# Optimization experiments

Hardware: AMD Instinct MI355X
Metric: run time of the kernel (lower is better)

## Reference

```python
import jax, jax.numpy as jnp
import numpy as np

N_NODES = 50000
N_EDGES = 600000
IN_C = 128
HID = 128
OUT_C = 32
N_GRAPHS = 64


def setup_inputs() -> dict:
    key = jax.random.key(0)
    ks = jax.random.split(key, 12)
    x = jax.random.normal(ks[0], (N_NODES, IN_C), dtype=jnp.float32)
    edge_index = jax.random.randint(ks[1], (2, N_EDGES), 0, N_NODES, dtype=jnp.int64)
    batch = jnp.sort(jax.random.randint(ks[2], (N_NODES,), 0, N_GRAPHS, dtype=jnp.int64))
    s1 = 1.0 / np.sqrt(IN_C)
    s2 = 1.0 / np.sqrt(HID)
    # SAGEConv: out = lin_l(mean_neighbors) + lin_r(x); lin_l has bias, lin_r has none
    W1l = jax.random.uniform(ks[3], (HID, IN_C), minval=-s1, maxval=s1, dtype=jnp.float32)
    b1 = jax.random.uniform(ks[4], (HID,), minval=-s1, maxval=s1, dtype=jnp.float32)
    W1r = jax.random.uniform(ks[5], (HID, IN_C), minval=-s1, maxval=s1, dtype=jnp.float32)
    W2l = jax.random.uniform(ks[6], (HID, HID), minval=-s2, maxval=s2, dtype=jnp.float32)
    b2 = jax.random.uniform(ks[7], (HID,), minval=-s2, maxval=s2, dtype=jnp.float32)
    W2r = jax.random.uniform(ks[8], (HID, HID), minval=-s2, maxval=s2, dtype=jnp.float32)
    Wlin = jax.random.uniform(ks[9], (OUT_C, HID), minval=-s2, maxval=s2, dtype=jnp.float32)
    blin = jax.random.uniform(ks[10], (OUT_C,), minval=-s2, maxval=s2, dtype=jnp.float32)
    return {"x": x, "edge_index": edge_index, "batch": batch,
            "W1l": W1l, "b1": b1, "W1r": W1r,
            "W2l": W2l, "b2": b2, "W2r": W2r,
            "Wlin": Wlin, "blin": blin}


def _sage_conv(x, src, dst, Wl, bl, Wr):
    # mean aggregation of source-node features onto destination nodes
    msg_sum = jax.ops.segment_sum(x[src], dst, num_segments=N_NODES)  # [N, d]
    deg = jax.ops.segment_sum(jnp.ones((src.shape[0],), x.dtype), dst, num_segments=N_NODES)
    mean = msg_sum / jnp.maximum(deg, 1.0)[:, None]
    return mean @ Wl.T + bl + x @ Wr.T


def reference(x, edge_index, batch, W1l, b1, W1r, W2l, b2, W2r, Wlin, blin):
    src, dst = edge_index[0], edge_index[1]
    h = jax.nn.relu(_sage_conv(x, src, dst, W1l, b1, W1r))
    h = jax.nn.relu(_sage_conv(h, src, dst, W2l, b2, W2r))
    # global mean pool over graph ids
    gsum = jax.ops.segment_sum(h, batch, num_segments=N_GRAPHS)        # [G, HID]
    cnt = jax.ops.segment_sum(jnp.ones((h.shape[0],), h.dtype), batch, num_segments=N_GRAPHS)
    pooled = gsum / jnp.maximum(cnt, 1.0)[:, None]
    return pooled @ Wlin.T + blin
```

## Files before the change

### kernel.cpp

```cpp
#include <hip/hip_runtime.h>
#include <hip/hip_fp16.h>

#define N_NODES 50000
#define N_EDGES 600000
#define N_GRAPHS 64
#define HID 128
#define OUT_C 32

#define N_SCAN_BLOCKS ((N_NODES + 255) / 256)
#define SCAN_FLAG 0x40000000

typedef __attribute__((ext_vector_type(8))) _Float16 half8;
typedef __attribute__((ext_vector_type(4))) float f32x4;

#define ZERO_INTS (2 * N_NODES + N_SCAN_BLOCKS + N_GRAPHS * HID)

__global__ __launch_bounds__(256) void zero_kernel(int* __restrict__ zb) {
    int i = blockIdx.x * 256 + threadIdx.x;
    if (i < ZERO_INTS) zb[i] = 0;
}

#define DEG_BLOCKS ((N_EDGES + 255) / 256)
#define GST_BLOCKS ((N_NODES + 256) / 256)

__global__ __launch_bounds__(256) void deg_gst_w(
    const int* __restrict__ dst, int* __restrict__ degi,
    const int* __restrict__ batch, int* __restrict__ gstart,
    const float* __restrict__ W1l, const float* __restrict__ W1r,
    const float* __restrict__ W2l, const float* __restrict__ W2r,
    __half* __restrict__ Wt1, __half* __restrict__ Wt2) {
    const int b = blockIdx.x;
    const int t = threadIdx.x;
    if (b < DEG_BLOCKS) {
        int e = b * 256 + t;
        if (e < N_EDGES) atomicAdd(&degi[dst[e]], 1);
    } else if (b < DEG_BLOCKS + GST_BLOCKS) {
        int i = (b - DEG_BLOCKS) * 256 + t;
        if (i <= N_NODES) {
            if (i == 0) {
                int b1 = batch[0];
                for (int g = 0; g <= b1; ++g) gstart[g] = 0;
            } else if (i == N_NODES) {
                int b0 = batch[N_NODES - 1];
                for (int g = b0 + 1; g <= N_GRAPHS; ++g) gstart[g] = N_NODES;
            } else {
                int b0 = batch[i - 1], b1 = batch[i];
                for (int g = b0 + 1; g <= b1; ++g) gstart[g] = i;
            }
        }
    } else {
        int local = (b - DEG_BLOCKS - GST_BLOCKS) * 256 + t;
        for (int i = local; i < 65536; i += 4096) {
            int which = i >> 15;
            int j = i & 32767;
            int n = j >> 8, k = j & 255;
            const float* Wl = which ? W2l : W1l;
            const float* Wr = which ? W2r : W1r;
            float a = (k < 128) ? Wl[n * 128 + k] : Wr[n * 128 + (k - 128)];
            (which ? Wt2 : Wt1)[j] = __float2half(a);
        }
    }
}

__global__ __launch_bounds__(256) void scan_fused(
    const int* __restrict__ deg, int* __restrict__ bsum,
    int* __restrict__ rowptr, float* __restrict__ invdeg) {
    __shared__ int s[256];
    const int b = blockIdx.x;
    const int t = threadIdx.x;
    const int idx = b * 256 + t;
    const int v = (idx < N_NODES) ? deg[idx] : 0;
    s[t] = v;
    __syncthreads();
    for (int off = 1; off < 256; off <<= 1) {
        int u = (t >= off) ? s[t - off] : 0;
        __syncthreads();
        s[t] += u;
        __syncthreads();
    }
    const int incl = s[t];
    if (t == 255) atomicExch(&bsum[b], incl | SCAN_FLAG);

    int pv = 0;
    if (t < b) {
        int w;
        do { w = atomicAdd(&bsum[t], 0); } while (!(w & SCAN_FLAG));
        pv = w & ~SCAN_FLAG;
    }
    __syncthreads();
    s[t] = pv;
    __syncthreads();
    for (int off = 128; off > 0; off >>= 1) {
        if (t < off) s[t] += s[t + off];
        __syncthreads();
    }
    const int boffs = s[0];

    if (idx < N_NODES) {
        rowptr[idx] = boffs + incl - v;
        invdeg[idx] = 1.0f / fmaxf((float)v, 1.0f);
    }
    if (b == N_SCAN_BLOCKS - 1 && t == 255) rowptr[N_NODES] = boffs + incl;
}

__global__ __launch_bounds__(256) void fill_cast(
    const int* __restrict__ src, const int* __restrict__ dst,
    const int* __restrict__ rowptr, int* __restrict__ cursor,
    int* __restrict__ eidx,
    const float* __restrict__ x, __half* __restrict__ xh) {
    const int b = blockIdx.x;
    const int t = threadIdx.x;
    if (b < DEG_BLOCKS) {
        int e = b * 256 + t;
        if (e < N_EDGES) {
            int d = dst[e];
            int pos = atomicAdd(&cursor[d], 1);
            eidx[rowptr[d] + pos] = src[e];
        }
    } else {
        int i = ((b - DEG_BLOCKS) * 256 + t) * 4;
        if (i < N_NODES * 128) {
            float4 v = *(const float4*)(x + i);
            __half2 a = __floats2half2_rn(v.x, v.y);
            __half2 c = __floats2half2_rn(v.z, v.w);
            uint2 st;
            st.x = *(const unsigned int*)&a;
            st.y = *(const unsigned int*)&c;
            *(uint2*)(xh + i) = st;
        }
    }
}

#define GBM 64

__global__ __launch_bounds__(256, 2) void sage_fused(
    const __half* __restrict__ feat16, const int* __restrict__ rowptr,
    const int* __restrict__ eidx, const float* __restrict__ invdeg,
    const __half* __restrict__ Wt, const float* __restrict__ bias,
    __half* __restrict__ out16,
    const int* __restrict__ batch, float* __restrict__ pooled,
    int M, int do_pool) {
    __shared__ __align__(16) __half Bs[128 * 256];
    __shared__ __align__(16) __half Ms[64 * 128];

    const int tid = threadIdx.x;
    const int wave = tid >> 6;
    const int lane = tid & 63;
    const int l15 = lane & 15;
    const int quad = lane >> 4;
    const int row0 = blockIdx.x * GBM;

    for (int id = tid; id < 128 * 32; id += 256) {
        int n = id >> 5;
        int kc16 = (id & 31) * 16;
        int off = (n * 512 + kc16) ^ ((n & 7) << 4);
        *(half8*)((char*)Bs + off) = *(const half8*)((const char*)Wt + n * 512 + kc16);
    }

    const int g16 = tid >> 4;
    const int sub = tid & 15;
    const int gbase = lane & 48;
    const size_t coff = (size_t)sub * 8;

    int begq[4], endq[4], pre0q[4], pre1q[4];
#pragma unroll
    for (int q = 0; q < 4; ++q) {
        int node = row0 + g16 + 16 * q;
        int bq = 0, eq = 0;
        if (node < M) { bq = rowptr[node]; eq = rowptr[node + 1]; }
        begq[q] = bq; endq[q] = eq;
    }
#pragma unroll
    for (int q = 0; q < 4; ++q) {
        int bq = begq[q], eq = endq[q];
        pre0q[q] = (eq > bq) ? eidx[min(bq + sub,      eq - 1)] : 0;
        pre1q[q] = (eq > bq) ? eidx[min(bq + 16 + sub, eq - 1)] : 0;
    }

#pragma unroll
    for (int q = 0; q < 4; ++q) {
        const int nloc = g16 + 16 * q;
        const int node = row0 + nloc;
        const int beg = begq[q], end = endq[q];
        const int deg = end - beg;

        float4 a[4], bb[4];
#pragma unroll
        for (int g = 0; g < 4; ++g) { a[g] = (float4){0.f,0.f,0.f,0.f}; bb[g] = (float4){0.f,0.f,0.f,0.f}; }

        for (int j0 = 0; j0 < deg; j0 += 16) {
            int idx[16];
            if (j0 == 0) {
#pragma unroll
                for (int k = 0; k < 16; ++k) idx[k] = __shfl(pre0q[q], gbase + k);
            } else if (j0 == 16) {
#pragma unroll
                for (int k = 0; k < 16; ++k) idx[k] = __shfl(pre1q[q], gbase + k);
            } else {
#pragma unroll
                for (int k = 0; k < 16; ++k) idx[k] = eidx[min(beg + j0 + k, end - 1)];
            }
            half8 v[16];
#pragma unroll
            for (int k = 0; k < 16; ++k)
                v[k] = *(const half8*)(feat16 + (size_t)idx[k] * 128 + coff);
            const int rem = deg - j0;
#pragma unroll
            for (int k = 0; k < 16; ++k) {
                const float w = (k < rem) ? 1.0f : 0.0f;
                const int g = k & 3;
                a[g].x  += w * (float)v[k][0];
                a[g].y  += w * (float)v[k][1];
                a[g].z  += w * (float)v[k][2];
                a[g].w  += w * (float)v[k][3];
                bb[g].x += w * (float)v[k][4];
                bb[g].y += w * (float)v[k][5];
                bb[g].z += w * (float)v[k][6];
                bb[g].w += w * (float)v[k][7];
            }
        }

        const float sc = (node < M) ? invdeg[node] : 1.0f;
        half8 r;
        r[0] = (_Float16)(((a[0].x + a[1].x) + (a[2].x + a[3].x)) * sc);
        r[1] = (_Float16)(((a[0].y + a[1].y) + (a[2].y + a[3].y)) * sc);
        r[2] = (_Float16)(((a[0].z + a[1].z) + (a[2].z + a[3].z)) * sc);
        r[3] = (_Float16)(((a[0].w + a[1].w) + (a[2].w + a[3].w)) * sc);
        r[4] = (_Float16)(((bb[0].x + bb[1].x) + (bb[2].x + bb[3].x)) * sc);
        r[5] = (_Float16)(((bb[0].y + bb[1].y) + (bb[2].y + bb[3].y)) * sc);
        r[6] = (_Float16)(((bb[0].z + bb[1].z) + (bb[2].z + bb[3].z)) * sc);
        r[7] = (_Float16)(((bb[0].w + bb[1].w) + (bb[2].w + bb[3].w)) * sc);
        int moff = (nloc * 256 + (int)sub * 16) ^ ((nloc & 7) << 4);
        *(half8*)((char*)Ms + moff) = r;
    }

    __syncthreads();

    const int arow = wave * 16 + l15;
    const int gi_a = min(row0 + arow, M - 1);
    half8 af[8];
#pragma unroll
    for (int kb = 0; kb < 4; ++kb) {
        int off = (arow * 256 + kb * 64 + quad * 16) ^ ((arow & 7) << 4);
        af[kb] = *(const half8*)((const char*)Ms + off);
    }
#pragma unroll
    for (int kb = 4; kb < 8; ++kb) {
        af[kb] = *(const half8*)(feat16 + (size_t)gi_a * 128 + (kb - 4) * 32 + quad * 8);
    }

    f32x4 acc[8];
#pragma unroll
    for (int t = 0; t < 8; ++t) acc[t] = (f32x4){0.f, 0.f, 0.f, 0.f};

#pragma unroll
    for (int kb = 0; kb < 8; ++kb) {
#pragma unroll
        for (int t = 0; t < 8; ++t) {
            const int n = t * 16 + l15;
            const int boff = (n * 512 + kb * 64 + quad * 16) ^ ((n & 7) << 4);
            const half8 b = *(const half8*)((const char*)Bs + boff);
            acc[t] = __builtin_amdgcn_mfma_f32_16x16x32_f16(af[kb], b, acc[t], 0, 0, 0);
        }
    }

    if (!do_pool) {
#pragma unroll
        for (int r = 0; r < 4; ++r) {
            int gi = row0 + wave * 16 + quad * 4 + r;
            if (gi < M) {
#pragma unroll
                for (int t = 0; t < 8; ++t) {
                    int col = t * 16 + l15;
                    float v = fmaxf(acc[t][r] + bias[col], 0.f);
                    out16[(size_t)gi * 128 + col] = __float2half(v);
                }
            }
        }
    } else {
        __syncthreads();
#pragma unroll
        for (int r = 0; r < 4; ++r) {
            int lrow = wave * 16 + quad * 4 + r;
            int gi = row0 + lrow;
#pragma unroll
            for (int t = 0; t < 8; ++t) {
                int col = t * 16 + l15;
                float v = fmaxf(acc[t][r] + bias[col], 0.f);
                if (gi >= M) v = 0.f;
                int off = (lrow * 256 + col * 2) ^ ((lrow & 7) << 4);
                *(__half*)((char*)Ms + off) = __float2half(v);
            }
        }
        __syncthreads();
        if (tid < 128) {
            const int col = tid;
            int cur = batch[min(row0, M - 1)];
            float s = 0.f;
            for (int r = 0; r < 64; ++r) {
                int gr = batch[min(row0 + r, M - 1)];
                if (gr != cur) {
                    atomicAdd(&pooled[cur * 128 + col], s);
                    s = 0.f; cur = gr;
                }
                int off = (r * 256 + col * 2) ^ ((r & 7) << 4);
                s += __half2float(*(const __half*)((const char*)Ms + off));
            }
            atomicAdd(&pooled[cur * 128 + col], s);
        }
    }
}

__global__ void final_kernel(const float* __restrict__ pooled,
                             const int* __restrict__ gstart,
                             const float* __restrict__ Wlin, const float* __restrict__ blin,
                             float* __restrict__ out) {
    int g = blockIdx.x;
    int j = threadIdx.x;
    float inv = 1.0f / fmaxf((float)(gstart[g + 1] - gstart[g]), 1.0f);
    float sum = blin[j];
    const float* w = Wlin + j * 128;
    const float* p = pooled + (size_t)g * 128;
    for (int c = 0; c < 128; ++c) {
        sum += p[c] * inv * w[c];
    }
    out[g * 32 + j] = sum;
}

extern "C" void kernel_launch(void* const* d_in, const int* in_sizes, int n_in,
                              void* d_out, int out_size, void* d_ws, size_t ws_size,
                              hipStream_t stream) {
    const float* x    = (const float*)d_in[0];
    const int*   src  = (const int*)d_in[1];
    const int*   dst  = ((const int*)d_in[1]) + N_EDGES;
    const int*   batch= (const int*)d_in[2];
    const float* W1l  = (const float*)d_in[3];
    const float* b1   = (const float*)d_in[4];
    const float* W1r  = (const float*)d_in[5];
    const float* W2l  = (const float*)d_in[6];
    const float* b2   = (const float*)d_in[7];
    const float* W2r  = (const float*)d_in[8];
    const float* Wlin = (const float*)d_in[9];
    const float* blin = (const float*)d_in[10];
    float* out = (float*)d_out;

    __half* xh     = (__half*)d_ws;
    __half* h1_16  = xh + 6400000;
    __half* Wt1    = h1_16 + 6400000;
    __half* Wt2    = Wt1 + 32768;
    float* invdeg  = (float*)(Wt2 + 32768);
    int*   gstart  = (int*)(invdeg + N_NODES);
    int*   degi    = gstart + 65;
    int*   cursor  = degi + N_NODES;
    int*   bsum    = cursor + N_NODES;
    float* pooled  = (float*)(bsum + N_SCAN_BLOCKS);
    int*   rowptr  = (int*)(pooled + N_GRAPHS*HID);
    int*   eidx    = rowptr + N_NODES + 1;

    zero_kernel<<<(ZERO_INTS + 255) / 256, 256, 0, stream>>>(degi);

    deg_gst_w<<<DEG_BLOCKS + GST_BLOCKS + 16, 256, 0, stream>>>(
        dst, degi, batch, gstart, W1l, W1r, W2l, W2r, Wt1, Wt2);

    scan_fused<<<N_SCAN_BLOCKS, 256, 0, stream>>>(degi, bsum, rowptr, invdeg);

    fill_cast<<<DEG_BLOCKS + (N_NODES * 128 / 4 + 255) / 256, 256, 0, stream>>>(
        src, dst, rowptr, cursor, eidx, x, xh);

    const int grid = (N_NODES + GBM - 1) / GBM;

    sage_fused<<<grid, 256, 0, stream>>>(
        xh, rowptr, eidx, invdeg, Wt1, b1, h1_16, batch, pooled, N_NODES, 0);

    sage_fused<<<grid, 256, 0, stream>>>(
        h1_16, rowptr, eidx, invdeg, Wt2, b2, (__half*)0, batch, pooled, N_NODES, 1);

    final_kernel<<<N_GRAPHS, 32, 0, stream>>>(pooled, gstart, Wlin, blin, out);
}
```

Before: 250.5 us.

## Make SAGE layers persistent with atomic 16-row tile scheduling; simplify scan lookback

Replaces the one-block-per-64-rows SAGE kernel with a persistent kernel of 512 blocks. Each block stages the weight matrix in LDS once, then pulls 16-row tiles from a global atomic counter, so weight loading is amortised and uneven node degrees are load-balanced dynamically. Each wave now computes 2 of the 8 output column tiles for a shared 16-row A tile. The scan kernel's decoupled lookback is also reduced to a single wave polling with sleep and a shuffle reduction, replacing the 256-thread LDS tree. Costs are an extra atomic and barrier per tile and smaller tiles per iteration. In the pooling path, output is written into the shared Ms buffer with no barrier after the A-fragment reads, so there is a possible cross-wave race.

```diff
diff --git a/kernel.cpp b/kernel.cpp
--- a/kernel.cpp
+++ b/kernel.cpp
@@ -9,11 +9,13 @@
 
 #define N_SCAN_BLOCKS ((N_NODES + 255) / 256)
 #define SCAN_FLAG 0x40000000
+#define N_TILES (N_NODES / 16)
+#define SAGE_BLOCKS 512
 
 typedef __attribute__((ext_vector_type(8))) _Float16 half8;
 typedef __attribute__((ext_vector_type(4))) float f32x4;
 
-#define ZERO_INTS (2 * N_NODES + N_SCAN_BLOCKS + N_GRAPHS * HID)
+#define ZERO_INTS (2 * N_NODES + N_SCAN_BLOCKS + N_GRAPHS * HID + 2)
 
 __global__ __launch_bounds__(256) void zero_kernel(int* __restrict__ zb) {
     int i = blockIdx.x * 256 + threadIdx.x;
@@ -82,18 +84,18 @@
     if (t == 255) atomicExch(&bsum[b], incl | SCAN_FLAG);
 
     int pv = 0;
-    if (t < b) {
-        int w;
-        do { w = atomicAdd(&bsum[t], 0); } while (!(w & SCAN_FLAG));
-        pv = w & ~SCAN_FLAG;
+    if (t < 64) {
+        for (int f = t; f < b; f += 64) {
+            int w;
+            while (!((w = atomicAdd(&bsum[f], 0)) & SCAN_FLAG)) {
+                __builtin_amdgcn_s_sleep(2);
+            }
+            pv += w & ~SCAN_FLAG;
+        }
+        for (int off = 32; off > 0; off >>= 1) pv += __shfl_down(pv, off);
+        if (t == 0) s[0] = pv;
     }
     __syncthreads();
-    s[t] = pv;
-    __syncthreads();
-    for (int off = 128; off > 0; off >>= 1) {
-        if (t < off) s[t] += s[t + off];
-        __syncthreads();
-    }
     const int boffs = s[0];
 
     if (idx < N_NODES) {
@@ -131,24 +133,22 @@
     }
 }
 
-#define GBM 64
-
-__global__ __launch_bounds__(256, 2) void sage_fused(
+__global__ __launch_bounds__(256, 2) void sage_persist(
     const __half* __restrict__ feat16, const int* __restrict__ rowptr,
     const int* __restrict__ eidx, const float* __restrict__ invdeg,
     const __half* __restrict__ Wt, const float* __restrict__ bias,
     __half* __restrict__ out16,
     const int* __restrict__ batch, float* __restrict__ pooled,
-    int M, int do_pool) {
+    int* __restrict__ ctr, int do_pool) {
     __shared__ __align__(16) __half Bs[128 * 256];
-    __shared__ __align__(16) __half Ms[64 * 128];
+    __shared__ __align__(16) __half Ms[16 * 128];
+    __shared__ int sTile;
 
     const int tid = threadIdx.x;
     const int wave = tid >> 6;
     const int lane = tid & 63;
     const int l15 = lane & 15;
     const int quad = lane >> 4;
-    const int row0 = blockIdx.x * GBM;
 
     for (int id = tid; id < 128 * 32; id += 256) {
         int n = id >> 5;
@@ -162,27 +162,19 @@
     const int gbase = lane & 48;
     const size_t coff = (size_t)sub * 8;
 
-    int begq[4], endq[4], pre0q[4], pre1q[4];
-#pragma unroll
-    for (int q = 0; q < 4; ++q) {
-        int node = row0 + g16 + 16 * q;
-        int bq = 0, eq = 0;
-        if (node < M) { bq = rowptr[node]; eq = rowptr[node + 1]; }
-        begq[q] = bq; endq[q] = eq;
-    }
-#pragma unroll
-    for (int q = 0; q < 4; ++q) {
-        int bq = begq[q], eq = endq[q];
-        pre0q[q] = (eq > bq) ? eidx[min(bq + sub,      eq - 1)] : 0;
-        pre1q[q] = (eq > bq) ? eidx[min(bq + 16 + sub, eq - 1)] : 0;
-    }
-
-#pragma unroll
-    for (int q = 0; q < 4; ++q) {
-        const int nloc = g16 + 16 * q;
-        const int node = row0 + nloc;
-        const int beg = begq[q], end = endq[q];
+    for (;;) {
+        if (tid == 0) sTile = atomicAdd(ctr, 1);
+        __syncthreads();
+        const int tile = sTile;
+        if (tile >= N_TILES) break;
+        const int row0 = tile * 16;
+
+        const int node = row0 + g16;
+        const int beg = rowptr[node];
+        const int end = rowptr[node + 1];
         const int deg = end - beg;
+        const int pre0 = (deg > 0) ? eidx[min(beg + sub,      end - 1)] : 0;
+        const int pre1 = (deg > 0) ? eidx[min(beg + 16 + sub, end - 1)] : 0;
 
         float4 a[4], bb[4];
 #pragma unroll
@@ -192,10 +184,10 @@
             int idx[16];
             if (j0 == 0) {
 #pragma unroll
-                for (int k = 0; k < 16; ++k) idx[k] = __shfl(pre0q[q], gbase + k);
+                for (int k = 0; k < 16; ++k) idx[k] = __shfl(pre0, gbase + k);
             } else if (j0 == 16) {
 #pragma unroll
-                for (int k = 0; k < 16; ++k) idx[k] = __shfl(pre1q[q], gbase + k);
+                for (int k = 0; k < 16; ++k) idx[k] = __shfl(pre1, gbase + k);
             } else {
 #pragma unroll
                 for (int k = 0; k < 16; ++k) idx[k] = eidx[min(beg + j0 + k, end - 1)];
@@ -220,7 +212,7 @@
             }
         }
 
-        const float sc = (node < M) ? invdeg[node] : 1.0f;
+        const float sc = invdeg[node];
         half8 r;
         r[0] = (_Float16)(((a[0].x + a[1].x) + (a[2].x + a[3].x)) * sc);
         r[1] = (_Float16)(((a[0].y + a[1].y) + (a[2].y + a[3].y)) * sc);
@@ -230,83 +222,76 @@
         r[5] = (_Float16)(((bb[0].y + bb[1].y) + (bb[2].y + bb[3].y)) * sc);
         r[6] = (_Float16)(((bb[0].z + bb[1].z) + (bb[2].z + bb[3].z)) * sc);
         r[7] = (_Float16)(((bb[0].w + bb[1].w) + (bb[2].w + bb[3].w)) * sc);
-        int moff = (nloc * 256 + (int)sub * 16) ^ ((nloc & 7) << 4);
+        int moff = (g16 * 256 + (int)sub * 16) ^ ((g16 & 7) << 4);
         *(half8*)((char*)Ms + moff) = r;
-    }
-
-    __syncthreads();
-
-    const int arow = wave * 16 + l15;
-    const int gi_a = min(row0 + arow, M - 1);
-    half8 af[8];
-#pragma unroll
-    for (int kb = 0; kb < 4; ++kb) {
-        int off = (arow * 256 + kb * 64 + quad * 16) ^ ((arow & 7) << 4);
-        af[kb] = *(const half8*)((const char*)Ms + off);
-    }
-#pragma unroll
-    for (int kb = 4; kb < 8; ++kb) {
-        af[kb] = *(const half8*)(feat16 + (size_t)gi_a * 128 + (kb - 4) * 32 + quad * 8);
-    }
-
-    f32x4 acc[8];
-#pragma unroll
-    for (int t = 0; t < 8; ++t) acc[t] = (f32x4){0.f, 0.f, 0.f, 0.f};
-
-#pragma unroll
-    for (int kb = 0; kb < 8; ++kb) {
-#pragma unroll
-        for (int t = 0; t < 8; ++t) {
-            const int n = t * 16 + l15;
-            const int boff = (n * 512 + kb * 64 + quad * 16) ^ ((n & 7) << 4);
-            const half8 b = *(const half8*)((const char*)Bs + boff);
-            acc[t] = __builtin_amdgcn_mfma_f32_16x16x32_f16(af[kb], b, acc[t], 0, 0, 0);
-        }
-    }
-
-    if (!do_pool) {
-#pragma unroll
-        for (int r = 0; r < 4; ++r) {
-            int gi = row0 + wave * 16 + quad * 4 + r;
-            if (gi < M) {
-#pragma unroll
-                for (int t = 0; t < 8; ++t) {
-                    int col = t * 16 + l15;
-                    float v = fmaxf(acc[t][r] + bias[col], 0.f);
+
+        __syncthreads();
+
+        half8 af[8];
+#pragma unroll
+        for (int kb = 0; kb < 4; ++kb) {
+            int off = (l15 * 256 + kb * 64 + quad * 16) ^ ((l15 & 7) << 4);
+            af[kb] = *(const half8*)((const char*)Ms + off);
+        }
+#pragma unroll
+        for (int kb = 4; kb < 8; ++kb) {
+            af[kb] = *(const half8*)(feat16 + (size_t)(row0 + l15) * 128 + (kb - 4) * 32 + quad * 8);
+        }
+
+        f32x4 acc[2];
+        acc[0] = (f32x4){0.f, 0.f, 0.f, 0.f};
+        acc[1] = (f32x4){0.f, 0.f, 0.f, 0.f};
+#pragma unroll
+        for (int tt = 0; tt < 2; ++tt) {
+            const int n = (wave * 2 + tt) * 16 + l15;
+#pragma unroll
+            for (int kb = 0; kb < 8; ++kb) {
+                const int boff = (n * 512 + kb * 64 + quad * 16) ^ ((n & 7) << 4);
+                const half8 b = *(const half8*)((const char*)Bs + boff);
+                acc[tt] = __builtin_amdgcn_mfma_f32_16x16x32_f16(af[kb], b, acc[tt], 0, 0, 0);
+            }
+        }
+
+        if (!do_pool) {
+#pragma unroll
+            for (int tt = 0; tt < 2; ++tt) {
+                const int col = (wave * 2 + tt) * 16 + l15;
+#pragma unroll
+                for (int rr = 0; rr < 4; ++rr) {
+                    const int gi = row0 + quad * 4 + rr;
+                    float v = fmaxf(acc[tt][rr] + bias[col], 0.f);
                     out16[(size_t)gi * 128 + col] = __float2half(v);
                 }
             }
-        }
-    } else {
-        __syncthreads();
-#pragma unroll
-        for (int r = 0; r < 4; ++r) {
-            int lrow = wave * 16 + quad * 4 + r;
-            int gi = row0 + lrow;
-#pragma unroll
-            for (int t = 0; t < 8; ++t) {
-                int col = t * 16 + l15;
-                float v = fmaxf(acc[t][r] + bias[col], 0.f);
-                if (gi >= M) v = 0.f;
-                int off = (lrow * 256 + col * 2) ^ ((lrow & 7) << 4);
-                *(__half*)((char*)Ms + off) = __float2half(v);
-            }
-        }
-        __syncthreads();
-        if (tid < 128) {
-            const int col = tid;
-            int cur = batch[min(row0, M - 1)];
-            float s = 0.f;
-            for (int r = 0; r < 64; ++r) {
-                int gr = batch[min(row0 + r, M - 1)];
-                if (gr != cur) {
-                    atomicAdd(&pooled[cur * 128 + col], s);
-                    s = 0.f; cur = gr;
+        } else {
+#pragma unroll
+            for (int tt = 0; tt < 2; ++tt) {
+                const int col = (wave * 2 + tt) * 16 + l15;
+#pragma unroll
+                for (int rr = 0; rr < 4; ++rr) {
+                    const int lrow = quad * 4 + rr;
+                    float v = fmaxf(acc[tt][rr] + bias[col], 0.f);
+                    int off = (lrow * 256 + col * 2) ^ ((lrow & 7) << 4);
+                    *(__half*)((char*)Ms + off) = __float2half(v);
                 }
-                int off = (r * 256 + col * 2) ^ ((r & 7) << 4);
-                s += __half2float(*(const __half*)((const char*)Ms + off));
-            }
-            atomicAdd(&pooled[cur * 128 + col], s);
+            }
+            __syncthreads();
+            if (tid < 128) {
+                const int col = tid;
+                int cur = batch[row0];
+                float s = 0.f;
+#pragma unroll
+                for (int rr = 0; rr < 16; ++rr) {
+                    int gr = batch[row0 + rr];
+                    if (gr != cur) {
+                        atomicAdd(&pooled[cur * 128 + col], s);
+                        s = 0.f; cur = gr;
+                    }
+                    int off = (rr * 256 + col * 2) ^ ((rr & 7) << 4);
+                    s += __half2float(*(const __half*)((const char*)Ms + off));
+                }
+                atomicAdd(&pooled[cur * 128 + col], s);
+            }
         }
     }
 }
@@ -354,7 +339,8 @@
     int*   cursor  = degi + N_NODES;
     int*   bsum    = cursor + N_NODES;
     float* pooled  = (float*)(bsum + N_SCAN_BLOCKS);
-    int*   rowptr  = (int*)(pooled + N_GRAPHS*HID);
+    int*   ctr     = (int*)(pooled + N_GRAPHS*HID);
+    int*   rowptr  = ctr + 2;
     int*   eidx    = rowptr + N_NODES + 1;
 
     zero_kernel<<<(ZERO_INTS + 255) / 256, 256, 0, stream>>>(degi);
@@ -367,13 +353,11 @@
     fill_cast<<<DEG_BLOCKS + (N_NODES * 128 / 4 + 255) / 256, 256, 0, stream>>>(
         src, dst, rowptr, cursor, eidx, x, xh);
 
-    const int grid = (N_NODES + GBM - 1) / GBM;
-
-    sage_fused<<<grid, 256, 0, stream>>>(
-        xh, rowptr, eidx, invdeg, Wt1, b1, h1_16, batch, pooled, N_NODES, 0);
-
-    sage_fused<<<grid, 256, 0, stream>>>(
-        h1_16, rowptr, eidx, invdeg, Wt2, b2, (__half*)0, batch, pooled, N_NODES, 1);
+    sage_persist<<<SAGE_BLOCKS, 256, 0, stream>>>(
+        xh, rowptr, eidx, invdeg, Wt1, b1, h1_16, batch, pooled, ctr + 0, 0);
+
+    sage_persist<<<SAGE_BLOCKS, 256, 0, stream>>>(
+        h1_16, rowptr, eidx, invdeg, Wt2, b2, (__half*)0, batch, pooled, ctr + 1, 1);
 
     final_kernel<<<N_GRAPHS, 32, 0, stream>>>(pooled, gstart, Wlin, blin, out);
 }
```

New measurement: 270.3 us. +7.9%, slower.

## Prefetch next node's first neighbor chunk and parallelize scan lookback

Applied to the files above, without the earlier changes.

The aggregation loop now loads the first 16 neighbor feature rows for the next node group while accumulating the current group, double-buffering gathers across the four per-thread nodes to hide memory latency. The decoupled-lookback scan now uses one wavefront striding over predecessor block sums, with a sleep while polling and a shuffle reduction, replacing the 256-thread shared-memory tree. The prefetch doubles the register footprint for gathered vectors (32 half8 values live), which may reduce occupancy or cause spills.

```diff
diff --git a/kernel.cpp b/kernel.cpp
--- a/kernel.cpp
+++ b/kernel.cpp
@@ -82,18 +82,18 @@
     if (t == 255) atomicExch(&bsum[b], incl | SCAN_FLAG);
 
     int pv = 0;
-    if (t < b) {
-        int w;
-        do { w = atomicAdd(&bsum[t], 0); } while (!(w & SCAN_FLAG));
-        pv = w & ~SCAN_FLAG;
+    if (t < 64) {
+        for (int f = t; f < b; f += 64) {
+            int w;
+            while (!((w = atomicAdd(&bsum[f], 0)) & SCAN_FLAG)) {
+                __builtin_amdgcn_s_sleep(2);
+            }
+            pv += w & ~SCAN_FLAG;
+        }
+        for (int off = 32; off > 0; off >>= 1) pv += __shfl_down(pv, off);
+        if (t == 0) s[0] = pv;
     }
     __syncthreads();
-    s[t] = pv;
-    __syncthreads();
-    for (int off = 128; off > 0; off >>= 1) {
-        if (t < off) s[t] += s[t + off];
-        __syncthreads();
-    }
     const int boffs = s[0];
 
     if (idx < N_NODES) {
@@ -177,6 +177,13 @@
         pre1q[q] = (eq > bq) ? eidx[min(bq + 16 + sub, eq - 1)] : 0;
     }
 
+    half8 vc[16];
+#pragma unroll
+    for (int k = 0; k < 16; ++k) {
+        int id0 = __shfl(pre0q[0], gbase + k);
+        vc[k] = *(const half8*)(feat16 + (size_t)id0 * 128 + coff);
+    }
+
 #pragma unroll
     for (int q = 0; q < 4; ++q) {
         const int nloc = g16 + 16 * q;
@@ -184,16 +191,36 @@
         const int beg = begq[q], end = endq[q];
         const int deg = end - beg;
 
+        half8 vn[16];
+        if (q < 3) {
+#pragma unroll
+            for (int k = 0; k < 16; ++k) {
+                int idn = __shfl(pre0q[q + 1], gbase + k);
+                vn[k] = *(const half8*)(feat16 + (size_t)idn * 128 + coff);
+            }
+        }
+
         float4 a[4], bb[4];
 #pragma unroll
         for (int g = 0; g < 4; ++g) { a[g] = (float4){0.f,0.f,0.f,0.f}; bb[g] = (float4){0.f,0.f,0.f,0.f}; }
 
-        for (int j0 = 0; j0 < deg; j0 += 16) {
+#pragma unroll
+        for (int k = 0; k < 16; ++k) {
+            const float w = (k < deg) ? 1.0f : 0.0f;
+            const int g = k & 3;
+            a[g].x  += w * (float)vc[k][0];
+            a[g].y  += w * (float)vc[k][1];
+            a[g].z  += w * (float)vc[k][2];
+            a[g].w  += w * (float)vc[k][3];
+            bb[g].x += w * (float)vc[k][4];
+            bb[g].y += w * (float)vc[k][5];
+            bb[g].z += w * (float)vc[k][6];
+            bb[g].w += w * (float)vc[k][7];
+        }
+
+        for (int j0 = 16; j0 < deg; j0 += 16) {
             int idx[16];
-            if (j0 == 0) {
-#pragma unroll
-                for (int k = 0; k < 16; ++k) idx[k] = __shfl(pre0q[q], gbase + k);
-            } else if (j0 == 16) {
+            if (j0 == 16) {
 #pragma unroll
                 for (int k = 0; k < 16; ++k) idx[k] = __shfl(pre1q[q], gbase + k);
             } else {
@@ -232,6 +259,11 @@
         r[7] = (_Float16)(((bb[0].w + bb[1].w) + (bb[2].w + bb[3].w)) * sc);
         int moff = (nloc * 256 + (int)sub * 16) ^ ((nloc & 7) << 4);
         *(half8*)((char*)Ms + moff) = r;
+
+        if (q < 3) {
+#pragma unroll
+            for (int k = 0; k < 16; ++k) vc[k] = vn[k];
+        }
     }
 
     __syncthreads();
```

Result: no change. 253.0 us (median of 2 runs) (+1.0%).
